# Kernel tuning notes

Hardware: AMD Instinct MI355X
Metric: run time of the kernel (lower is better)

## Reference

```python
import jax, jax.numpy as jnp
import numpy as np

B, L, LE = 2, 1024, 1024
NM, DM, NL = 80, 512, 8
LAYERS = NL // 2
DS, EXP, K, H = 16, 2, 4, 4
DI = EXP * DM            # 1024
DTR = (DM + 15) // 16    # dt_rank 'auto' -> 32
HD = DM // H             # 128


def setup_inputs() -> dict:
    key = jax.random.key(0)
    ks = iter(jax.random.split(key, 48))
    n = lambda shape, s=0.02: jax.random.normal(next(ks), shape, jnp.float32) * s
    return {
        "x": jax.random.normal(next(ks), (B, L, NM), jnp.float32),
        "enc_output": jax.random.normal(next(ks), (B, LE, DM), jnp.float32),
        "W_in": n((DM, NM)), "b_in": jnp.zeros((DM,), jnp.float32),
        "m_norm_w": jnp.ones((LAYERS, DM), jnp.float32),
        "m_in_w": n((LAYERS, 2 * DI, DM)),
        "m_conv_w": n((LAYERS, DI, K), 0.1),
        "m_conv_b": jnp.zeros((LAYERS, DI), jnp.float32),
        "m_xproj_w": n((LAYERS, DTR + 2 * DS, DI)),
        "m_dt_w": n((LAYERS, DI, DTR)),
        "m_dt_b": n((LAYERS, DI), 0.1),
        "m_Alog": jnp.tile(jnp.log(jnp.arange(1, DS + 1, dtype=jnp.float32))[None, None, :], (LAYERS, DI, 1)),
        "m_D": jnp.ones((LAYERS, DI), jnp.float32),
        "m_out_w": n((LAYERS, DM, DI)),
        "a_in_w": n((LAYERS, 3 * DM, DM)),
        "a_in_b": jnp.zeros((LAYERS, 3 * DM), jnp.float32),
        "a_out_w": n((LAYERS, DM, DM)),
        "a_out_b": jnp.zeros((LAYERS, DM), jnp.float32),
        "a_ln_w": jnp.ones((LAYERS, DM), jnp.float32),
        "a_ln_b": jnp.zeros((LAYERS, DM), jnp.float32),
        "normf_w": jnp.ones((DM,), jnp.float32),
        "W_out": n((NM, DM)),
    }


def rmsnorm(x, w, eps=1e-5):
    return x * jax.lax.rsqrt(jnp.mean(x * x, axis=-1, keepdims=True) + eps) * w


def layernorm(x, w, b, eps=1e-5):
    m = jnp.mean(x, axis=-1, keepdims=True)
    v = jnp.mean((x - m) ** 2, axis=-1, keepdims=True)
    return (x - m) * jax.lax.rsqrt(v + eps) * w + b


def dwconv_causal(x, w, b):
    # x: (B,L,DI), w: (DI,K) depthwise; torch Conv1d(padding=K-1)[..., :L] == left-pad K-1
    xt = jnp.transpose(x, (0, 2, 1))  # (B,DI,L)
    y = jax.lax.conv_general_dilated(xt, w[:, None, :], (1,), [(K - 1, 0)],
                                     feature_group_count=DI,
                                     dimension_numbers=("NCH", "OIH", "NCH"))
    return jnp.transpose(y, (0, 2, 1)) + b


def selective_scan_cumsum(u, delta, A, Bm, Cm, Dv):
    # mamba-tiny 'cumsum' scan. u,delta: (B,L,DI); A: (DI,DS); Bm,Cm: (B,L,DS); Dv: (DI,)
    dA = jnp.einsum("bld,dn->bldn", delta, A)
    dBu = jnp.einsum("bld,bld,bln->bldn", delta, u, Bm)
    shifted = jnp.pad(dA[:, 1:], ((0, 0), (0, 1), (0, 0), (0, 0)))
    dA_cs = jnp.exp(jnp.flip(jnp.cumsum(jnp.flip(shifted, 1), 1), 1))  # suffix-sum exp
    xs = jnp.cumsum(dBu * dA_cs, axis=1) / (dA_cs + 1e-12)
    y = jnp.einsum("bldn,bln->bld", xs, Cm)
    return y + u * Dv


def mamba_block(u, in_w, conv_w, conv_b, xproj_w, dt_w, dt_b, Alog, Dv, out_w):
    xr = u @ in_w.T                       # (B,L,2*DI)
    xm, res = xr[..., :DI], xr[..., DI:]
    xm = jax.nn.silu(dwconv_causal(xm, conv_w, conv_b))
    x_dbl = xm @ xproj_w.T                # (B,L,DTR+2*DS)
    dlt = x_dbl[..., :DTR]
    Bm = x_dbl[..., DTR:DTR + DS]
    Cm = x_dbl[..., DTR + DS:]
    delta = jax.nn.softplus(dlt @ dt_w.T + dt_b)
    A = -jnp.exp(Alog)
    y = selective_scan_cumsum(xm, delta, A, Bm, Cm, Dv)
    y = y * jax.nn.silu(res)
    return y @ out_w.T


def cross_attn_block(q_in, kv, in_w, in_b, out_w, out_b, ln_w, ln_b):
    Wq, Wk, Wv = in_w[:DM], in_w[DM:2 * DM], in_w[2 * DM:]
    bq, bk, bv = in_b[:DM], in_b[DM:2 * DM], in_b[2 * DM:]
    q = (q_in @ Wq.T + bq).reshape(B, -1, H, HD)
    k = (kv @ Wk.T + bk).reshape(B, -1, H, HD)
    v = (kv @ Wv.T + bv).reshape(B, -1, H, HD)
    scores = jnp.einsum("bqhd,bkhd->bhqk", q, k) / jnp.sqrt(jnp.float32(HD))
    attn = jax.nn.softmax(scores, axis=-1)
    o = jnp.einsum("bhqk,bkhd->bqhd", attn, v).reshape(B, -1, DM)
    o = o @ out_w.T + out_b
    return layernorm(q_in + o, ln_w, ln_b)  # dropout is identity in eval


def reference(x, enc_output, W_in, b_in, m_norm_w, m_in_w, m_conv_w, m_conv_b,
              m_xproj_w, m_dt_w, m_dt_b, m_Alog, m_D, m_out_w,
              a_in_w, a_in_b, a_out_w, a_out_b, a_ln_w, a_ln_b, normf_w, W_out):
    h = x @ W_in.T + b_in
    for i in range(LAYERS):
        h = h + mamba_block(rmsnorm(h, m_norm_w[i]), m_in_w[i], m_conv_w[i],
                            m_conv_b[i], m_xproj_w[i], m_dt_w[i], m_dt_b[i],
                            m_Alog[i], m_D[i], m_out_w[i])
        h = cross_attn_block(h, enc_output, a_in_w[i], a_in_b[i],
                             a_out_w[i], a_out_b[i], a_ln_w[i], a_ln_b[i])
    h = rmsnorm(h, normf_w)
    return h @ W_out.T
```

## Files before the change

kernel.cpp:

```cpp
#include <hip/hip_runtime.h>
#include <hip/hip_bf16.h>
#include <math.h>

typedef __hip_bfloat16 bf16;
typedef __attribute__((ext_vector_type(8))) short short8x;
typedef __attribute__((ext_vector_type(4))) float f32x4;

static constexpr int cB   = 2;
static constexpr int cL   = 1024;
static constexpr int cLE  = 1024;
static constexpr int cNM  = 80;
static constexpr int cDM  = 512;
static constexpr int cLAYERS = 4;
static constexpr int cDS  = 16;
static constexpr int cKC  = 4;
static constexpr int cH   = 4;
static constexpr int cDI  = 1024;
static constexpr int cDTR = 32;
static constexpr int cHD  = 128;

static constexpr int cNCH = 64;
static constexpr int cCHL = cL / cNCH;
static constexpr int cSPL = 4;

#define GLL16(g, l) __builtin_amdgcn_global_load_lds( \
    (const __attribute__((address_space(1))) void*)(g), \
    (__attribute__((address_space(3))) void*)(l), 16, 0, 0)

template<int ACT, int BM, int BN>
__global__ __launch_bounds__(256)
void bgemm_kernel(const bf16* __restrict__ A, const bf16* __restrict__ W,
                  const float* __restrict__ bias, const float* __restrict__ addv,
                  float* __restrict__ Cf, bf16* __restrict__ Cb,
                  int M, int N, int Kd, int lda, int ldw, int ldcf, int ldcb, int ldadd,
                  int bdiv, long sA1, long sA2, long sW1, long sW2,
                  long sCf1, long sCf2, long sCb1, long sCb2, long sBias)
{
    constexpr int RM = BM / 32;
    constexpr int RN = BN / 32;
    const int z = blockIdx.z;
    const int i1 = z / bdiv, i2 = z % bdiv;
    A += i1 * sA1 + i2 * sA2;
    W += i1 * sW1 + i2 * sW2;
    if (bias) bias += i1 * sBias;

    const int bm = blockIdx.y * BM;
    const int bn = blockIdx.x * BN;
    const int tid = threadIdx.x;
    const int lane = tid & 63;
    const int wid = tid >> 6;
    const int wr = wid >> 1, wc = wid & 1;

    __shared__ bf16 As[BM * 32];
    __shared__ bf16 Bs[BN * 32];

    f32x4 acc[RM][RN] = {};

    const int r_in = lane >> 2;
    const int kb   = (lane & 3) * 8;
    const int hi   = lane >> 4;
    const int rc   = lane & 15;

    for (int k0 = 0; k0 < Kd; k0 += 32) {
#pragma unroll
        for (int iss = 0; iss < BM / 64; iss++) {
            const int row = wid * (BM / 4) + iss * 16 + r_in;
            int gm = bm + row; if (gm >= M) gm = M - 1;
            const bf16* ga = A + (long)gm * lda + k0 + kb;
            GLL16(ga, As + (wid * (BM / 4) + iss * 16) * 32);
        }
#pragma unroll
        for (int iss = 0; iss < BN / 64; iss++) {
            const int row = wid * (BN / 4) + iss * 16 + r_in;
            int gn = bn + row; if (gn >= N) gn = N - 1;
            const bf16* gb = W + (long)gn * ldw + k0 + kb;
            GLL16(gb, Bs + (wid * (BN / 4) + iss * 16) * 32);
        }
        asm volatile("s_waitcnt vmcnt(0)" ::: "memory");
        __syncthreads();

        short8x af[RM], bfv[RN];
#pragma unroll
        for (int i = 0; i < RM; i++)
            af[i] = *(const short8x*)(As + (wr * (BM / 2) + i * 16 + rc) * 32 + hi * 8);
#pragma unroll
        for (int j = 0; j < RN; j++)
            bfv[j] = *(const short8x*)(Bs + (wc * (BN / 2) + j * 16 + rc) * 32 + hi * 8);
#pragma unroll
        for (int i = 0; i < RM; i++)
#pragma unroll
            for (int j = 0; j < RN; j++)
                acc[i][j] = __builtin_amdgcn_mfma_f32_16x16x32_bf16(af[i], bfv[j], acc[i][j], 0, 0, 0);
        __syncthreads();
    }

    const long cfo = i1 * sCf1 + i2 * sCf2;
    const long cbo = i1 * sCb1 + i2 * sCb2;
#pragma unroll
    for (int i = 0; i < RM; i++) {
#pragma unroll
        for (int r = 0; r < 4; r++) {
            const int gm = bm + wr * (BM / 2) + i * 16 + hi * 4 + r;
            if (gm >= M) continue;
#pragma unroll
            for (int j = 0; j < RN; j++) {
                const int gn = bn + wc * (BN / 2) + j * 16 + rc;
                if (gn >= N) continue;
                float v = acc[i][j][r];
                if (bias) v += bias[gn];
                if (ACT == 1) v = (v > 20.f) ? v : log1pf(__expf(v));
                if (addv) v += addv[cfo + (long)gm * ldadd + gn];
                if (Cf) Cf[cfo + (long)gm * ldcf + gn] = v;
                if (Cb) Cb[cbo + (long)gm * ldcb + gn] = __float2bfloat16(v);
            }
        }
    }
}

static inline void bgemm(int ACT, int BM, int BN, const bf16* A, const bf16* W, const float* bias,
                         const float* addv, float* Cf, bf16* Cb,
                         int M, int N, int Kd, int lda, int ldw, int ldcf, int ldcb, int ldadd,
                         int nz, int bdiv, long sA1, long sA2, long sW1, long sW2,
                         long sCf1, long sCf2, long sCb1, long sCb2, long sBias, hipStream_t s)
{
    dim3 g((N + BN - 1) / BN, (M + BM - 1) / BM, nz), b(256);
#define BG_ARGS A, W, bias, addv, Cf, Cb, M, N, Kd, lda, ldw, ldcf, ldcb, ldadd, \
                bdiv, sA1, sA2, sW1, sW2, sCf1, sCf2, sCb1, sCb2, sBias
    if (BM == 128) {
        if (ACT == 1) bgemm_kernel<1, 128, 128><<<g, b, 0, s>>>(BG_ARGS);
        else          bgemm_kernel<0, 128, 128><<<g, b, 0, s>>>(BG_ARGS);
    } else if (BN == 128) {
        if (ACT == 1) bgemm_kernel<1, 64, 128><<<g, b, 0, s>>>(BG_ARGS);
        else          bgemm_kernel<0, 64, 128><<<g, b, 0, s>>>(BG_ARGS);
    } else {
        bgemm_kernel<0, 64, 64><<<g, b, 0, s>>>(BG_ARGS);
    }
#undef BG_ARGS
}

static inline void bgemm_plain(int ACT, int BM, int BN, const bf16* A, const bf16* W,
                               const float* bias, const float* addv, float* Cf, bf16* Cb,
                               int M, int N, int Kd, int lda, int ldw, int ldcf, int ldcb,
                               int ldadd, hipStream_t s)
{
    bgemm(ACT, BM, BN, A, W, bias, addv, Cf, Cb, M, N, Kd, lda, ldw, ldcf, ldcb, ldadd,
          1, 1, 0, 0, 0, 0, 0, 0, 0, 0, 0, s);
}

__global__ __launch_bounds__(128)
void flash_split_kernel(const bf16* __restrict__ Qp, const bf16* __restrict__ Kp,
                        const bf16* __restrict__ VTp, float* __restrict__ OP,
                        float2* __restrict__ ML, float scale)
{
    const int qt = blockIdx.x;
    const int bh = blockIdx.y;
    const int sp = blockIdx.z;
    const int b = bh >> 2, h = bh & 3;
    const int tid = threadIdx.x;
    const int w = tid >> 6;
    const int lane = tid & 63;
    const int rc = lane & 15, hi = lane >> 4;
    const int rlo = rc & 7;

    __shared__ bf16 Ks[64 * 128];
    __shared__ bf16 Vs[128 * 64];
    __shared__ bf16 Ps[32 * 64];

    {
        const bf16* qb = Qp + ((long)(b * cL + qt * 32)) * cDM + h * cHD;
#pragma unroll
        for (int c = 0; c < 4; c++) {
            const int row = w * 16 + c * 4 + (lane >> 4);
            const int gc = (lane & 15) ^ (row & 7);
            GLL16(qb + (long)row * cDM + gc * 8, Ks + (w * 16 + c * 4) * 128);
        }
    }
    asm volatile("s_waitcnt vmcnt(0)" ::: "memory");
    __syncthreads();
    short8x aq[4];
#pragma unroll
    for (int kk = 0; kk < 4; kk++) {
        const int sc = (kk * 4 + hi) ^ rlo;
        aq[kk] = *(const short8x*)(Ks + (w * 16 + rc) * 128 + sc * 8);
    }
    __syncthreads();

    float m_r[4], l_r[4];
#pragma unroll
    for (int r = 0; r < 4; r++) { m_r[r] = -1e30f; l_r[r] = 0.f; }
    f32x4 oacc[8] = {};

    const bf16* kb0 = Kp + ((long)(b * cLE)) * (2 * cDM) + h * cHD;
    const bf16* vb0 = VTp + ((long)(b * cDM + h * cHD)) * cLE;

    for (int t = 0; t < 4; t++) {
        const int kt = sp * 4 + t;
        __syncthreads();
#pragma unroll
        for (int c = 0; c < 8; c++) {
            const int row = w * 32 + c * 4 + (lane >> 4);
            const int gc = (lane & 15) ^ (row & 7);
            GLL16(kb0 + ((long)(kt * 64 + row)) * (2 * cDM) + gc * 8,
                  Ks + (w * 32 + c * 4) * 128);
        }
#pragma unroll
        for (int c = 0; c < 8; c++) {
            const int row = w * 64 + c * 8 + (lane >> 3);
            const int gc = (lane & 7) ^ (row & 7);
            GLL16(vb0 + (long)row * cLE + kt * 64 + gc * 8,
                  Vs + (w * 64 + c * 8) * 64);
        }
        asm volatile("s_waitcnt vmcnt(0)" ::: "memory");
        __syncthreads();

        f32x4 s[4] = {};
#pragma unroll
        for (int kk = 0; kk < 4; kk++) {
            const int sc = (kk * 4 + hi) ^ rlo;
#pragma unroll
            for (int j = 0; j < 4; j++) {
                short8x bk = *(const short8x*)(Ks + (j * 16 + rc) * 128 + sc * 8);
                s[j] = __builtin_amdgcn_mfma_f32_16x16x32_bf16(aq[kk], bk, s[j], 0, 0, 0);
            }
        }

        float p[4][4];
        float esc[4];
#pragma unroll
        for (int r = 0; r < 4; r++) {
            const float v0 = s[0][r] * scale, v1 = s[1][r] * scale;
            const float v2 = s[2][r] * scale, v3 = s[3][r] * scale;
            float mx = fmaxf(fmaxf(v0, v1), fmaxf(v2, v3));
            mx = fmaxf(mx, __shfl_xor(mx, 1));
            mx = fmaxf(mx, __shfl_xor(mx, 2));
            mx = fmaxf(mx, __shfl_xor(mx, 4));
            mx = fmaxf(mx, __shfl_xor(mx, 8));
            const float mn = fmaxf(m_r[r], mx);
            p[0][r] = __expf(v0 - mn);
            p[1][r] = __expf(v1 - mn);
            p[2][r] = __expf(v2 - mn);
            p[3][r] = __expf(v3 - mn);
            float rs = (p[0][r] + p[1][r]) + (p[2][r] + p[3][r]);
            rs += __shfl_xor(rs, 1);
            rs += __shfl_xor(rs, 2);
            rs += __shfl_xor(rs, 4);
            rs += __shfl_xor(rs, 8);
            esc[r] = __expf(m_r[r] - mn);
            l_r[r] = l_r[r] * esc[r] + rs;
            m_r[r] = mn;
        }
#pragma unroll
        for (int j2 = 0; j2 < 8; j2++)
#pragma unroll
            for (int r = 0; r < 4; r++)
                oacc[j2][r] *= esc[r];
#pragma unroll
        for (int j = 0; j < 4; j++)
#pragma unroll
            for (int r = 0; r < 4; r++) {
                const int q = w * 16 + hi * 4 + r;
                const int cp = (j * 2 + (rc >> 3)) ^ (q & 7);
                Ps[q * 64 + cp * 8 + (rc & 7)] = __float2bfloat16(p[j][r]);
            }
        __syncthreads();
#pragma unroll
        for (int ks = 0; ks < 2; ks++) {
            const int sc = (ks * 4 + hi) ^ rlo;
            short8x ap = *(const short8x*)(Ps + (w * 16 + rc) * 64 + sc * 8);
#pragma unroll
            for (int j2 = 0; j2 < 8; j2++) {
                short8x bv = *(const short8x*)(Vs + (j2 * 16 + rc) * 64 + sc * 8);
                oacc[j2] = __builtin_amdgcn_mfma_f32_16x16x32_bf16(ap, bv, oacc[j2], 0, 0, 0);
            }
        }
    }

    float* ob = OP + (((long)sp * (cB * cL) + b * cL + qt * 32)) * cDM + h * cHD;
#pragma unroll
    for (int j2 = 0; j2 < 8; j2++)
#pragma unroll
        for (int r = 0; r < 4; r++)
            ob[(long)(w * 16 + hi * 4 + r) * cDM + j2 * 16 + rc] = oacc[j2][r];
    if (rc == 0) {
#pragma unroll
        for (int r = 0; r < 4; r++) {
            const int row = qt * 32 + w * 16 + hi * 4 + r;
            ML[(((long)sp * cB + b) * cH + h) * cL + row] = make_float2(m_r[r], l_r[r]);
        }
    }
}

__global__ __launch_bounds__(256)
void flash_combine_kernel(const float* __restrict__ OP, const float2* __restrict__ ML,
                          bf16* __restrict__ Op)
{
    const int row = blockIdx.x;
    const int b = row >> 10, lr = row & 1023;
    const int t = threadIdx.x;
    __shared__ float ms[cSPL][cH], ls[cSPL][cH];
    __shared__ float wgt[cSPL][cH], linv[cH];
    if (t < cSPL * cH) {
        const int s = t >> 2, h = t & 3;
        float2 v = ML[(((long)s * cB + b) * cH + h) * cL + lr];
        ms[s][h] = v.x; ls[s][h] = v.y;
    }
    __syncthreads();
    if (t < cH) {
        const int h = t;
        float M = fmaxf(fmaxf(ms[0][h], ms[1][h]), fmaxf(ms[2][h], ms[3][h]));
        float L = 0.f;
#pragma unroll
        for (int s = 0; s < cSPL; s++) {
            const float e = __expf(ms[s][h] - M);
            wgt[s][h] = e;
            L += e * ls[s][h];
        }
        linv[h] = 1.f / L;
    }
    __syncthreads();
#pragma unroll
    for (int c0 = 0; c0 < 2; c0++) {
        const int col = t + c0 * 256;
        const int h = col >> 7;
        float o = 0.f;
#pragma unroll
        for (int s = 0; s < cSPL; s++)
            o += wgt[s][h] * OP[((long)s * (cB * cL) + row) * cDM + col];
        Op[(long)row * cDM + col] = __float2bfloat16(o * linv[h]);
    }
}

__global__ void splitk_reduce_kernel(const float* __restrict__ parts, float* __restrict__ outf,
                                     bf16* __restrict__ outb, int n4, int sliceN4, int S)
{
    const int i = blockIdx.x * 256 + threadIdx.x;
    if (i >= n4) return;
    float4 a = ((const float4*)parts)[i];
    for (int s2 = 1; s2 < S; s2++) {
        float4 b2 = ((const float4*)parts)[i + (long)s2 * sliceN4];
        a.x += b2.x; a.y += b2.y; a.z += b2.z; a.w += b2.w;
    }
    ((float4*)outf)[i] = a;
    bf16 b0 = __float2bfloat16(a.x), b1 = __float2bfloat16(a.y);
    bf16 b2 = __float2bfloat16(a.z), b3 = __float2bfloat16(a.w);
    short4 pk = { *(short*)&b0, *(short*)&b1, *(short*)&b2, *(short*)&b3 };
    ((short4*)outb)[i] = pk;
}

__global__ void cvt_all_kernel(
    const float* __restrict__ s0, bf16* __restrict__ d0,
    const float* __restrict__ s1, bf16* __restrict__ d1,
    const float* __restrict__ s2, bf16* __restrict__ d2,
    const float* __restrict__ s3, bf16* __restrict__ d3,
    const float* __restrict__ s4, bf16* __restrict__ d4,
    const float* __restrict__ s5, bf16* __restrict__ d5,
    const float* __restrict__ s6, bf16* __restrict__ d6,
    const float* __restrict__ s7, bf16* __restrict__ d7)
{
    constexpr long E0 = 1048576, E1 = 4194304, E2 = 262144, E3 = 131072;
    constexpr long E4 = 2097152, E5 = 3145728, E6 = 1048576, E7 = 40960;
    constexpr long C0 = E0, C1 = C0 + E1, C2 = C1 + E2, C3 = C2 + E3;
    constexpr long C4 = C3 + E4, C5 = C4 + E5, C6 = C5 + E6, C7 = C6 + E7;
    long i = ((long)blockIdx.x * 256 + threadIdx.x) * 4;
    if (i >= C7) return;
    const float* s; bf16* d;
    if      (i < C0) { s = s0; d = d0; }
    else if (i < C1) { s = s1; d = d1; i -= C0; }
    else if (i < C2) { s = s2; d = d2; i -= C1; }
    else if (i < C3) { s = s3; d = d3; i -= C2; }
    else if (i < C4) { s = s4; d = d4; i -= C3; }
    else if (i < C5) { s = s5; d = d5; i -= C4; }
    else if (i < C6) { s = s6; d = d6; i -= C5; }
    else             { s = s7; d = d7; i -= C6; }
    float4 v = *(const float4*)(s + i);
    d[i]     = __float2bfloat16(v.x);
    d[i + 1] = __float2bfloat16(v.y);
    d[i + 2] = __float2bfloat16(v.z);
    d[i + 3] = __float2bfloat16(v.w);
}

__global__ void cvt_pad_kernel(const float* __restrict__ in, bf16* __restrict__ out,
                               int rows, int kin, int kout)
{
    const int idx = blockIdx.x * 256 + threadIdx.x;
    if (idx >= rows * kout) return;
    const int r = idx / kout, k = idx - r * kout;
    out[idx] = __float2bfloat16(k < kin ? in[(long)r * kin + k] : 0.f);
}

__global__ void transpose_bf16_kernel(const bf16* __restrict__ in, bf16* __restrict__ out,
                                      int ldin, int col0, long inLS, long outLS)
{
    __shared__ bf16 t[32][33];
    const int z = blockIdx.z;
    const int lay = z >> 1, b = z & 1;
    in  += (long)lay * inLS;
    out += (long)lay * outLS;
    const int le0 = blockIdx.x * 32, d0 = blockIdx.y * 32;
    const int tid = threadIdx.x;
    const int c = tid & 31, r = tid >> 5;
    for (int i = r; i < 32; i += 8)
        t[i][c] = in[((long)b * cLE + le0 + i) * ldin + col0 + d0 + c];
    __syncthreads();
    for (int i = r; i < 32; i += 8)
        out[((long)b * cDM + d0 + i) * cLE + le0 + c] = t[c][i];
}

__global__ void rmsnorm_kernel(const float* __restrict__ x, const float* __restrict__ w,
                               float* __restrict__ outf, bf16* __restrict__ outb, int Dm)
{
    const int row = blockIdx.x;
    const float* xr = x + (long)row * Dm;
    float s = 0.f;
    for (int i = threadIdx.x; i < Dm; i += 256) { float v = xr[i]; s += v * v; }
    __shared__ float red[5];
    const int lane = threadIdx.x & 63, wv = threadIdx.x >> 6;
#pragma unroll
    for (int off = 1; off < 64; off <<= 1) s += __shfl_xor(s, off);
    if (lane == 0) red[wv] = s;
    __syncthreads();
    if (threadIdx.x == 0) {
        float t = red[0] + red[1] + red[2] + red[3];
        red[4] = rsqrtf(t / Dm + 1e-5f);
    }
    __syncthreads();
    const float scale = red[4];
    for (int i = threadIdx.x; i < Dm; i += 256) {
        float v = xr[i] * scale * w[i];
        if (outf) outf[(long)row * Dm + i] = v;
        if (outb) outb[(long)row * Dm + i] = __float2bfloat16(v);
    }
}

__global__ void layernorm_kernel(const float* __restrict__ x, const float* __restrict__ w,
                                 const float* __restrict__ b, float* __restrict__ outf,
                                 bf16* __restrict__ outb,
                                 const float* __restrict__ rms_w, bf16* __restrict__ rms_out)
{
    const int row = blockIdx.x;
    const float* xr = x + (long)row * 512;
    const int t = threadIdx.x;
    const int i0 = t, i1 = t + 256;
    float x0 = xr[i0], x1 = xr[i1];
    float s = x0 + x1, sq = x0 * x0 + x1 * x1;
    __shared__ float red[8];
    __shared__ float mv[2];
    const int lane = t & 63, wv = t >> 6;
#pragma unroll
    for (int off = 1; off < 64; off <<= 1) { s += __shfl_xor(s, off); sq += __shfl_xor(sq, off); }
    if (lane == 0) { red[wv] = s; red[4 + wv] = sq; }
    __syncthreads();
    if (t == 0) {
        float ts = red[0] + red[1] + red[2] + red[3];
        float tq = red[4] + red[5] + red[6] + red[7];
        float m = ts / 512.f;
        float var = tq / 512.f - m * m;
        mv[0] = m;
        mv[1] = rsqrtf(var + 1e-5f);
    }
    __syncthreads();
    const float m = mv[0], rs = mv[1];
    const float v0 = (x0 - m) * rs * w[i0] + b[i0];
    const float v1 = (x1 - m) * rs * w[i1] + b[i1];
    outf[(long)row * 512 + i0] = v0;
    outf[(long)row * 512 + i1] = v1;
    outb[(long)row * 512 + i0] = __float2bfloat16(v0);
    outb[(long)row * 512 + i1] = __float2bfloat16(v1);
    float s2 = v0 * v0 + v1 * v1;
#pragma unroll
    for (int off = 1; off < 64; off <<= 1) s2 += __shfl_xor(s2, off);
    if (lane == 0) red[wv] = s2;
    __syncthreads();
    if (t == 0) mv[0] = rsqrtf((red[0] + red[1] + red[2] + red[3]) / 512.f + 1e-5f);
    __syncthreads();
    const float rsc = mv[0];
    rms_out[(long)row * 512 + i0] = __float2bfloat16(v0 * rsc * rms_w[i0]);
    rms_out[(long)row * 512 + i1] = __float2bfloat16(v1 * rsc * rms_w[i1]);
}

__global__ void conv_silu_kernel(const float* __restrict__ xr, const float* __restrict__ w,
                                 const float* __restrict__ bias, float* __restrict__ xm,
                                 bf16* __restrict__ xmb)
{
    const int idx = blockIdx.x * 256 + threadIdx.x;
    if (idx >= cB * cL * cDI) return;
    const int d = idx & (cDI - 1);
    const int l = (idx >> 10) & (cL - 1);
    const int b = idx >> 20;
    float s = bias[d];
#pragma unroll
    for (int j = 0; j < cKC; j++) {
        const int ls = l + j - (cKC - 1);
        if (ls >= 0) s += w[d * cKC + j] * xr[((long)(b * cL + ls)) * (2 * cDI) + d];
    }
    s = s / (1.f + __expf(-s));
    xm[(long)idx] = s;
    xmb[(long)idx] = __float2bfloat16(s);
}

__global__ void scan_phase1(const float* __restrict__ xm, const float* __restrict__ delta,
                            const float* __restrict__ xdbl, const float* __restrict__ Alog,
                            float* __restrict__ aprod_out, float* __restrict__ send_out)
{
    const int idx4 = blockIdx.x * 256 + threadIdx.x;
    const int ng = idx4 & 3;
    const int d  = (idx4 >> 2) & (cDI - 1);
    const int ch = (idx4 >> 12) & (cNCH - 1);
    const int b  = idx4 >> 18;
    const float4 Al = *(const float4*)(Alog + d * cDS + 4 * ng);
    const float A0 = -__expf(Al.x), A1 = -__expf(Al.y), A2 = -__expf(Al.z), A3 = -__expf(Al.w);
    float s0 = 0.f, s1 = 0.f, s2 = 0.f, s3 = 0.f;
    float p0 = 1.f, p1 = 1.f, p2 = 1.f, p3 = 1.f;
    const int l0 = ch * cCHL;
    const float* dp = delta + (long)(b * cL + l0) * cDI + d;
    const float* up = xm    + (long)(b * cL + l0) * cDI + d;
    const float* xb = xdbl  + (long)(b * cL + l0) * 64 + cDTR + 4 * ng;
#pragma unroll
    for (int t = 0; t < cCHL; t++) {
        const float dl = dp[(long)t * cDI];
        const float du = dl * up[(long)t * cDI];
        const float4 Bv = *(const float4*)(xb + (long)t * 64);
        const float a0 = __expf(dl * A0), a1 = __expf(dl * A1);
        const float a2 = __expf(dl * A2), a3 = __expf(dl * A3);
        s0 = a0 * s0 + du * Bv.x; p0 *= a0;
        s1 = a1 * s1 + du * Bv.y; p1 *= a1;
        s2 = a2 * s2 + du * Bv.z; p2 *= a2;
        s3 = a3 * s3 + du * Bv.w; p3 *= a3;
    }
    const long base4 = (((long)(b * cNCH + ch) * cDI + d) * cDS) + 4 * ng;
    float4 pv = { p0, p1, p2, p3 };
    float4 sv = { s0, s1, s2, s3 };
    *(float4*)(aprod_out + base4) = pv;
    *(float4*)(send_out + base4)  = sv;
}

__global__ void scan_phase2(const float* __restrict__ aprod, const float* __restrict__ send,
                            float* __restrict__ sinit)
{
    const int j = blockIdx.x * 64 + threadIdx.x;
    const int n = j & (cDS - 1);
    const int d = (j >> 4) & (cDI - 1);
    const int b = j >> 14;
    float s = 0.f;
#pragma unroll
    for (int c = 0; c < cNCH; c++) {
        const long off = (((long)(b * cNCH + c) * cDI + d) * cDS) + n;
        sinit[off] = s;
        s = aprod[off] * s + send[off];
    }
}

__global__ void scan_phase3(const float* __restrict__ xm, const float* __restrict__ delta,
                            const float* __restrict__ xdbl, const float* __restrict__ Alog,
                            const float* __restrict__ Dv, const float* __restrict__ xr,
                            const float* __restrict__ sinit, bf16* __restrict__ y)
{
    const int idx4 = blockIdx.x * 256 + threadIdx.x;
    const int ng = idx4 & 3;
    const int d  = (idx4 >> 2) & (cDI - 1);
    const int ch = (idx4 >> 12) & (cNCH - 1);
    const int b  = idx4 >> 18;
    const float4 Al = *(const float4*)(Alog + d * cDS + 4 * ng);
    const float A0 = -__expf(Al.x), A1 = -__expf(Al.y), A2 = -__expf(Al.z), A3 = -__expf(Al.w);
    const float Dval = Dv[d];
    const long base4 = (((long)(b * cNCH + ch) * cDI + d) * cDS) + 4 * ng;
    float4 st = *(const float4*)(sinit + base4);
    float s0 = st.x, s1 = st.y, s2 = st.z, s3 = st.w;
    const int l0 = ch * cCHL;
    const float* dp = delta + (long)(b * cL + l0) * cDI + d;
    const float* up = xm    + (long)(b * cL + l0) * cDI + d;
    const float* xb = xdbl  + (long)(b * cL + l0) * 64 + cDTR + 4 * ng;
    const float* xc = xb + cDS;
    const float* rp = xr + (long)(b * cL + l0) * (2 * cDI) + cDI + d;
    bf16* yp = y + (long)(b * cL + l0) * cDI + d;
#pragma unroll
    for (int t = 0; t < cCHL; t++) {
        const float dl = dp[(long)t * cDI];
        const float u  = up[(long)t * cDI];
        const float du = dl * u;
        const float4 Bv = *(const float4*)(xb + (long)t * 64);
        const float4 Cv = *(const float4*)(xc + (long)t * 64);
        const float a0 = __expf(dl * A0), a1 = __expf(dl * A1);
        const float a2 = __expf(dl * A2), a3 = __expf(dl * A3);
        s0 = a0 * s0 + du * Bv.x;
        s1 = a1 * s1 + du * Bv.y;
        s2 = a2 * s2 + du * Bv.z;
        s3 = a3 * s3 + du * Bv.w;
        float c = s0 * Cv.x;
        c = fmaf(s1, Cv.y, c);
        c = fmaf(s2, Cv.z, c);
        c = fmaf(s3, Cv.w, c);
        c += __shfl_xor(c, 1);
        c += __shfl_xor(c, 2);
        if (ng == 0) {
            const float res = rp[(long)t * 2 * cDI];
            const float sig = 1.f / (1.f + __expf(-res));
            yp[(long)t * cDI] = __float2bfloat16((c + u * Dval) * (res * sig));
        }
    }
}

extern "C" void kernel_launch(void* const* d_in, const int* in_sizes, int n_in,
                              void* d_out, int out_size, void* d_ws, size_t ws_size,
                              hipStream_t stream)
{
    const float* x       = (const float*)d_in[0];
    const float* enc     = (const float*)d_in[1];
    const float* W_in    = (const float*)d_in[2];
    const float* b_in    = (const float*)d_in[3];
    const float* m_norm_w= (const float*)d_in[4];
    const float* m_in_w  = (const float*)d_in[5];
    const float* m_conv_w= (const float*)d_in[6];
    const float* m_conv_b= (const float*)d_in[7];
    const float* m_xproj = (const float*)d_in[8];
    const float* m_dt_w  = (const float*)d_in[9];
    const float* m_dt_b  = (const float*)d_in[10];
    const float* m_Alog  = (const float*)d_in[11];
    const float* m_D     = (const float*)d_in[12];
    const float* m_out_w = (const float*)d_in[13];
    const float* a_in_w  = (const float*)d_in[14];
    const float* a_in_b  = (const float*)d_in[15];
    const float* a_out_w = (const float*)d_in[16];
    const float* a_out_b = (const float*)d_in[17];
    const float* a_ln_w  = (const float*)d_in[18];
    const float* a_ln_b  = (const float*)d_in[19];
    const float* normf_w = (const float*)d_in[20];
    const float* W_out   = (const float*)d_in[21];
    float* out = (float*)d_out;

    float* ws = (float*)d_ws;
    long off = 0;
    auto allocf = [&](long n) { float* p = ws + off; off += n; return p; };

    const long M1 = 1 << 20;
    float* bufH    = allocf(M1);
    float* bufPre  = allocf(M1);
    float* bufXR   = allocf(4 * M1);
    float* bufXM   = allocf(2 * M1);
    float* bufDelta= allocf(2 * M1);
    float* bufXDBL = allocf(M1 / 8);
    bf16* bufU    = (bf16*)allocf(M1 / 2);
    bf16* bufHb   = (bf16*)allocf(M1 / 2);
    bf16* bufXMb  = (bf16*)allocf(M1);
    bf16* bufXDBLb= (bf16*)allocf(M1 / 16);
    bf16* bufY    = (bf16*)allocf(M1);
    bf16* bufQ    = (bf16*)allocf(M1 / 2);
    bf16* bufO    = (bf16*)allocf(M1 / 2);
    bf16* encb    = (bf16*)allocf(M1 / 2);
    bf16* w_in_b  = (bf16*)allocf(2 * M1);
    bf16* w_xp_b  = (bf16*)allocf(M1 / 8);
    bf16* w_dt_b  = (bf16*)allocf(M1 / 16);
    bf16* w_out_b = (bf16*)allocf(M1);
    bf16* w_ain_b = (bf16*)allocf(3 * M1 / 2);
    bf16* w_aout_b= (bf16*)allocf(M1 / 2);
    bf16* x_pad   = (bf16*)allocf(2048L * 96 / 2);
    bf16* w_inp_b = (bf16*)allocf(512L * 96 / 2);
    bf16* w_outf_b= (bf16*)allocf(80L * 512 / 2);
    float* bufAP  = allocf(2 * M1);
    float* bufSE  = allocf(2 * M1);
    float* bufSI  = allocf(2 * M1);
    bf16* bufKV4  = (bf16*)allocf(4 * M1);
    bf16* bufVT4  = (bf16*)allocf(2 * M1);
    float* bufOP  = allocf(4 * M1);
    float2* bufML = (float2*)allocf(M1 / 16);

    const int Mrows = cB * cL;
    const long SUMSZ4 = (long)cB * cNCH * cDI * 4;
    const long kvLS = (long)Mrows * 2 * cDM;
    const long vtLS = (long)cB * cDM * cLE;

    cvt_all_kernel<<<11688, 256, 0, stream>>>(
        enc, encb, m_in_w, w_in_b, m_xproj, w_xp_b, m_dt_w, w_dt_b,
        m_out_w, w_out_b, a_in_w, w_ain_b, a_out_w, w_aout_b, W_out, w_outf_b);
    cvt_pad_kernel<<<(Mrows * 96 + 255) / 256, 256, 0, stream>>>(x, x_pad, Mrows, cNM, 96);
    cvt_pad_kernel<<<(cDM * 96 + 255) / 256, 256, 0, stream>>>(W_in, w_inp_b, cDM, cNM, 96);

    bgemm(0, 64, 128, encb, w_ain_b + (long)cDM * cDM, a_in_b + cDM, nullptr, nullptr, bufKV4,
          Mrows, 2 * cDM, cDM, cDM, cDM, 0, 2 * cDM, 0,
          cLAYERS, 1,
          0, 0,
          (long)3 * cDM * cDM, 0,
          0, 0, kvLS, 0,
          (long)3 * cDM,
          stream);
    {
        dim3 g(cLE / 32, cDM / 32, cLAYERS * cB);
        transpose_bf16_kernel<<<g, 256, 0, stream>>>(bufKV4, bufVT4, 2 * cDM, cDM, kvLS, vtLS);
    }

    bgemm_plain(0, 64, 64, x_pad, w_inp_b, b_in, nullptr, bufH, nullptr,
                Mrows, cDM, 96, 96, 96, cDM, 0, 0, stream);
    rmsnorm_kernel<<<Mrows, 256, 0, stream>>>(bufH, m_norm_w, nullptr, bufU, cDM);

    for (int i = 0; i < cLAYERS; i++) {
        const bf16*  in_w   = w_in_b   + (long)i * 2 * cDI * cDM;
        const float* conv_w = m_conv_w + (long)i * cDI * cKC;
        const float* conv_b = m_conv_b + (long)i * cDI;
        const bf16*  xproj  = w_xp_b   + (long)i * 64 * cDI;
        const bf16*  dt_w   = w_dt_b   + (long)i * cDI * cDTR;
        const float* dt_b   = m_dt_b   + (long)i * cDI;
        const float* Alog   = m_Alog   + (long)i * cDI * cDS;
        const float* Dv     = m_D      + (long)i * cDI;
        const bf16*  out_w  = w_out_b  + (long)i * cDM * cDI;
        const bf16*  ain_w  = w_ain_b  + (long)i * 3 * cDM * cDM;
        const float* ain_b  = a_in_b   + (long)i * 3 * cDM;
        const bf16*  aout_w = w_aout_b + (long)i * cDM * cDM;
        const float* aout_b = a_out_b  + (long)i * cDM;
        const float* ln_w   = a_ln_w   + (long)i * cDM;
        const float* ln_b   = a_ln_b   + (long)i * cDM;
        const bf16*  kv_l   = bufKV4 + (long)i * kvLS;
        const bf16*  vt_l   = bufVT4 + (long)i * vtLS;
        const float* next_rms_w = (i + 1 < cLAYERS) ? (m_norm_w + (long)(i + 1) * cDM) : normf_w;

        bgemm_plain(0, 64, 128, bufU, in_w, nullptr, nullptr, bufXR, nullptr,
                    Mrows, 2 * cDI, cDM, cDM, cDM, 2 * cDI, 0, 0, stream);
        conv_silu_kernel<<<(cB * cL * cDI) / 256, 256, 0, stream>>>(bufXR, conv_w, conv_b, bufXM, bufXMb);
        bgemm(0, 64, 64, bufXMb, xproj, nullptr, nullptr, bufPre, nullptr,
              Mrows, 64, cDI / 8, cDI, cDI, 64, 0, 0,
              8, 1, 128, 0, 128, 0, (long)Mrows * 64, 0, 0, 0, 0, stream);
        splitk_reduce_kernel<<<(Mrows * 64 / 4 + 255) / 256, 256, 0, stream>>>(
            bufPre, bufXDBL, bufXDBLb, Mrows * 64 / 4, Mrows * 64 / 4, 8);
        bgemm_plain(1, 64, 128, bufXDBLb, dt_w, dt_b, nullptr, bufDelta, nullptr,
                    Mrows, cDI, cDTR, 64, cDTR, cDI, 0, 0, stream);
        scan_phase1<<<(int)(SUMSZ4 / 256), 256, 0, stream>>>(bufXM, bufDelta, bufXDBL, Alog, bufAP, bufSE);
        scan_phase2<<<(cB * cDI * cDS) / 64, 64, 0, stream>>>(bufAP, bufSE, bufSI);
        scan_phase3<<<(int)(SUMSZ4 / 256), 256, 0, stream>>>(bufXM, bufDelta, bufXDBL, Alog, Dv, bufXR, bufSI, bufY);
        bgemm_plain(0, 64, 64, bufY, out_w, nullptr, bufH, bufH, bufHb,
                    Mrows, cDM, cDI, cDI, cDI, cDM, cDM, cDM, stream);

        bgemm_plain(0, 64, 64, bufHb, ain_w, ain_b, nullptr, nullptr, bufQ,
                    Mrows, cDM, cDM, cDM, cDM, 0, cDM, 0, stream);
        {
            dim3 g(cL / 32, cB * cH, cSPL);
            flash_split_kernel<<<g, 128, 0, stream>>>(bufQ, kv_l, vt_l, bufOP, bufML,
                                                      0.08838834764831845f);
        }
        flash_combine_kernel<<<Mrows, 256, 0, stream>>>(bufOP, bufML, bufO);
        bgemm_plain(0, 64, 64, bufO, aout_w, aout_b, bufH, bufPre, nullptr,
                    Mrows, cDM, cDM, cDM, cDM, cDM, 0, cDM, stream);
        layernorm_kernel<<<Mrows, 256, 0, stream>>>(bufPre, ln_w, ln_b, bufH, bufHb,
                                                    next_rms_w, bufU);
    }

    bgemm_plain(0, 64, 64, bufU, w_outf_b, nullptr, nullptr, out, nullptr,
                Mrows, cNM, cDM, cDM, cDM, cNM, 0, 0, stream);
}
```

Before: 741.1 us.

## Fuse three chunked selective-scan phases into one kernel with shared-memory prefix scan

```diff
diff --git a/kernel.cpp b/kernel.cpp
--- a/kernel.cpp
+++ b/kernel.cpp
@@ -498,23 +498,33 @@
     xmb[(long)idx] = __float2bfloat16(s);
 }
 
-__global__ void scan_phase1(const float* __restrict__ xm, const float* __restrict__ delta,
-                            const float* __restrict__ xdbl, const float* __restrict__ Alog,
-                            float* __restrict__ aprod_out, float* __restrict__ send_out)
-{
-    const int idx4 = blockIdx.x * 256 + threadIdx.x;
-    const int ng = idx4 & 3;
-    const int d  = (idx4 >> 2) & (cDI - 1);
-    const int ch = (idx4 >> 12) & (cNCH - 1);
-    const int b  = idx4 >> 18;
+__global__ __launch_bounds__(256)
+void scan_fused_kernel(const float* __restrict__ xm, const float* __restrict__ delta,
+                       const float* __restrict__ xdbl, const float* __restrict__ Alog,
+                       const float* __restrict__ Dv, const float* __restrict__ xr,
+                       bf16* __restrict__ y)
+{
+    const int blk = blockIdx.x;
+    const int d = blk & (cDI - 1);
+    const int b = blk >> 10;
+    const int tid = threadIdx.x;
+    const int ch = tid >> 2;
+    const int ng = tid & 3;
+
     const float4 Al = *(const float4*)(Alog + d * cDS + 4 * ng);
     const float A0 = -__expf(Al.x), A1 = -__expf(Al.y), A2 = -__expf(Al.z), A3 = -__expf(Al.w);
-    float s0 = 0.f, s1 = 0.f, s2 = 0.f, s3 = 0.f;
-    float p0 = 1.f, p1 = 1.f, p2 = 1.f, p3 = 1.f;
+    const float Dval = Dv[d];
+
     const int l0 = ch * cCHL;
     const float* dp = delta + (long)(b * cL + l0) * cDI + d;
     const float* up = xm    + (long)(b * cL + l0) * cDI + d;
     const float* xb = xdbl  + (long)(b * cL + l0) * 64 + cDTR + 4 * ng;
+    const float* xc = xb + cDS;
+    const float* rp = xr + (long)(b * cL + l0) * (2 * cDI) + cDI + d;
+    bf16* yp = y + (long)(b * cL + l0) * cDI + d;
+
+    float s0 = 0.f, s1 = 0.f, s2 = 0.f, s3 = 0.f;
+    float p0 = 1.f, p1 = 1.f, p2 = 1.f, p3 = 1.f;
 #pragma unroll
     for (int t = 0; t < cCHL; t++) {
         const float dl = dp[(long)t * cDI];
@@ -527,52 +537,45 @@
         s2 = a2 * s2 + du * Bv.z; p2 *= a2;
         s3 = a3 * s3 + du * Bv.w; p3 *= a3;
     }
-    const long base4 = (((long)(b * cNCH + ch) * cDI + d) * cDS) + 4 * ng;
-    float4 pv = { p0, p1, p2, p3 };
-    float4 sv = { s0, s1, s2, s3 };
-    *(float4*)(aprod_out + base4) = pv;
-    *(float4*)(send_out + base4)  = sv;
-}
-
-__global__ void scan_phase2(const float* __restrict__ aprod, const float* __restrict__ send,
-                            float* __restrict__ sinit)
-{
-    const int j = blockIdx.x * 64 + threadIdx.x;
-    const int n = j & (cDS - 1);
-    const int d = (j >> 4) & (cDI - 1);
-    const int b = j >> 14;
-    float s = 0.f;
-#pragma unroll
-    for (int c = 0; c < cNCH; c++) {
-        const long off = (((long)(b * cNCH + c) * cDI + d) * cDS) + n;
-        sinit[off] = s;
-        s = aprod[off] * s + send[off];
-    }
-}
-
-__global__ void scan_phase3(const float* __restrict__ xm, const float* __restrict__ delta,
-                            const float* __restrict__ xdbl, const float* __restrict__ Alog,
-                            const float* __restrict__ Dv, const float* __restrict__ xr,
-                            const float* __restrict__ sinit, bf16* __restrict__ y)
-{
-    const int idx4 = blockIdx.x * 256 + threadIdx.x;
-    const int ng = idx4 & 3;
-    const int d  = (idx4 >> 2) & (cDI - 1);
-    const int ch = (idx4 >> 12) & (cNCH - 1);
-    const int b  = idx4 >> 18;
-    const float4 Al = *(const float4*)(Alog + d * cDS + 4 * ng);
-    const float A0 = -__expf(Al.x), A1 = -__expf(Al.y), A2 = -__expf(Al.z), A3 = -__expf(Al.w);
-    const float Dval = Dv[d];
-    const long base4 = (((long)(b * cNCH + ch) * cDI + d) * cDS) + 4 * ng;
-    float4 st = *(const float4*)(sinit + base4);
-    float s0 = st.x, s1 = st.y, s2 = st.z, s3 = st.w;
-    const int l0 = ch * cCHL;
-    const float* dp = delta + (long)(b * cL + l0) * cDI + d;
-    const float* up = xm    + (long)(b * cL + l0) * cDI + d;
-    const float* xb = xdbl  + (long)(b * cL + l0) * 64 + cDTR + 4 * ng;
-    const float* xc = xb + cDS;
-    const float* rp = xr + (long)(b * cL + l0) * (2 * cDI) + cDI + d;
-    bf16* yp = y + (long)(b * cL + l0) * cDI + d;
+
+    __shared__ float As[cNCH][17], Ss[cNCH][17];
+    As[ch][4 * ng + 0] = p0; Ss[ch][4 * ng + 0] = s0;
+    As[ch][4 * ng + 1] = p1; Ss[ch][4 * ng + 1] = s1;
+    As[ch][4 * ng + 2] = p2; Ss[ch][4 * ng + 2] = s2;
+    As[ch][4 * ng + 3] = p3; Ss[ch][4 * ng + 3] = s3;
+    __syncthreads();
+    for (int st = 1; st < cNCH; st <<= 1) {
+        float na[4], nb[4];
+        const bool act = (ch >= st);
+        if (act) {
+#pragma unroll
+            for (int j = 0; j < 4; j++) {
+                const int n = 4 * ng + j;
+                const float ah = As[ch][n], bh = Ss[ch][n];
+                na[j] = ah * As[ch - st][n];
+                nb[j] = ah * Ss[ch - st][n] + bh;
+            }
+        }
+        __syncthreads();
+        if (act) {
+#pragma unroll
+            for (int j = 0; j < 4; j++) {
+                const int n = 4 * ng + j;
+                As[ch][n] = na[j];
+                Ss[ch][n] = nb[j];
+            }
+        }
+        __syncthreads();
+    }
+    if (ch > 0) {
+        s0 = Ss[ch - 1][4 * ng + 0];
+        s1 = Ss[ch - 1][4 * ng + 1];
+        s2 = Ss[ch - 1][4 * ng + 2];
+        s3 = Ss[ch - 1][4 * ng + 3];
+    } else {
+        s0 = s1 = s2 = s3 = 0.f;
+    }
+
 #pragma unroll
     for (int t = 0; t < cCHL; t++) {
         const float dl = dp[(long)t * cDI];
@@ -656,16 +659,12 @@
     bf16* x_pad   = (bf16*)allocf(2048L * 96 / 2);
     bf16* w_inp_b = (bf16*)allocf(512L * 96 / 2);
     bf16* w_outf_b= (bf16*)allocf(80L * 512 / 2);
-    float* bufAP  = allocf(2 * M1);
-    float* bufSE  = allocf(2 * M1);
-    float* bufSI  = allocf(2 * M1);
     bf16* bufKV4  = (bf16*)allocf(4 * M1);
     bf16* bufVT4  = (bf16*)allocf(2 * M1);
     float* bufOP  = allocf(4 * M1);
     float2* bufML = (float2*)allocf(M1 / 16);
 
     const int Mrows = cB * cL;
-    const long SUMSZ4 = (long)cB * cNCH * cDI * 4;
     const long kvLS = (long)Mrows * 2 * cDM;
     const long vtLS = (long)cB * cDM * cLE;
 
@@ -722,9 +721,8 @@
             bufPre, bufXDBL, bufXDBLb, Mrows * 64 / 4, Mrows * 64 / 4, 8);
         bgemm_plain(1, 64, 128, bufXDBLb, dt_w, dt_b, nullptr, bufDelta, nullptr,
                     Mrows, cDI, cDTR, 64, cDTR, cDI, 0, 0, stream);
-        scan_phase1<<<(int)(SUMSZ4 / 256), 256, 0, stream>>>(bufXM, bufDelta, bufXDBL, Alog, bufAP, bufSE);
-        scan_phase2<<<(cB * cDI * cDS) / 64, 64, 0, stream>>>(bufAP, bufSE, bufSI);
-        scan_phase3<<<(int)(SUMSZ4 / 256), 256, 0, stream>>>(bufXM, bufDelta, bufXDBL, Alog, Dv, bufXR, bufSI, bufY);
+        scan_fused_kernel<<<cB * cDI, 256, 0, stream>>>(bufXM, bufDelta, bufXDBL, Alog, Dv,
+                                                        bufXR, bufY);
         bgemm_plain(0, 64, 64, bufY, out_w, nullptr, bufH, bufH, bufHb,
                     Mrows, cDM, cDI, cDI, cDI, cDM, cDM, cDM, stream);
 
```

Result: slower. 912.2 us (+23.1%).

## Give each scan thread all 16 states and vectorize conv-silu by four channels

Applied to the files above, without the earlier changes.

```diff
diff --git a/kernel.cpp b/kernel.cpp
--- a/kernel.cpp
+++ b/kernel.cpp
@@ -483,55 +483,82 @@
                                  bf16* __restrict__ xmb)
 {
     const int idx = blockIdx.x * 256 + threadIdx.x;
-    if (idx >= cB * cL * cDI) return;
-    const int d = idx & (cDI - 1);
-    const int l = (idx >> 10) & (cL - 1);
-    const int b = idx >> 20;
-    float s = bias[d];
+    const int d4 = idx & (cDI / 4 - 1);
+    const int l  = (idx >> 8) & (cL - 1);
+    const int b  = idx >> 18;
+    const int d  = d4 * 4;
+    float4 acc = *(const float4*)(bias + d);
+    float w0a[4], w1a[4], w2a[4], w3a[4];
+    *(float4*)w0a = *(const float4*)(w + (d + 0) * cKC);
+    *(float4*)w1a = *(const float4*)(w + (d + 1) * cKC);
+    *(float4*)w2a = *(const float4*)(w + (d + 2) * cKC);
+    *(float4*)w3a = *(const float4*)(w + (d + 3) * cKC);
 #pragma unroll
     for (int j = 0; j < cKC; j++) {
         const int ls = l + j - (cKC - 1);
-        if (ls >= 0) s += w[d * cKC + j] * xr[((long)(b * cL + ls)) * (2 * cDI) + d];
-    }
-    s = s / (1.f + __expf(-s));
-    xm[(long)idx] = s;
-    xmb[(long)idx] = __float2bfloat16(s);
-}
-
-__global__ void scan_phase1(const float* __restrict__ xm, const float* __restrict__ delta,
-                            const float* __restrict__ xdbl, const float* __restrict__ Alog,
-                            float* __restrict__ aprod_out, float* __restrict__ send_out)
-{
-    const int idx4 = blockIdx.x * 256 + threadIdx.x;
-    const int ng = idx4 & 3;
-    const int d  = (idx4 >> 2) & (cDI - 1);
-    const int ch = (idx4 >> 12) & (cNCH - 1);
-    const int b  = idx4 >> 18;
-    const float4 Al = *(const float4*)(Alog + d * cDS + 4 * ng);
-    const float A0 = -__expf(Al.x), A1 = -__expf(Al.y), A2 = -__expf(Al.z), A3 = -__expf(Al.w);
-    float s0 = 0.f, s1 = 0.f, s2 = 0.f, s3 = 0.f;
-    float p0 = 1.f, p1 = 1.f, p2 = 1.f, p3 = 1.f;
+        if (ls >= 0) {
+            const float4 xv = *(const float4*)(xr + ((long)(b * cL + ls)) * (2 * cDI) + d);
+            acc.x = fmaf(w0a[j], xv.x, acc.x);
+            acc.y = fmaf(w1a[j], xv.y, acc.y);
+            acc.z = fmaf(w2a[j], xv.z, acc.z);
+            acc.w = fmaf(w3a[j], xv.w, acc.w);
+        }
+    }
+    acc.x = acc.x / (1.f + __expf(-acc.x));
+    acc.y = acc.y / (1.f + __expf(-acc.y));
+    acc.z = acc.z / (1.f + __expf(-acc.z));
+    acc.w = acc.w / (1.f + __expf(-acc.w));
+    const long o = ((long)(b * cL + l)) * cDI + d;
+    *(float4*)(xm + o) = acc;
+    bf16 b0 = __float2bfloat16(acc.x), b1 = __float2bfloat16(acc.y);
+    bf16 b2 = __float2bfloat16(acc.z), b3 = __float2bfloat16(acc.w);
+    short4 pk = { *(short*)&b0, *(short*)&b1, *(short*)&b2, *(short*)&b3 };
+    *(short4*)(xmb + o) = pk;
+}
+
+__global__ __launch_bounds__(256)
+void scan_phase1(const float* __restrict__ xm, const float* __restrict__ delta,
+                 const float* __restrict__ xdbl, const float* __restrict__ Alog,
+                 float* __restrict__ aprod_out, float* __restrict__ send_out)
+{
+    const int idx = blockIdx.x * 256 + threadIdx.x;
+    const int d  = idx & (cDI - 1);
+    const int ch = (idx >> 10) & (cNCH - 1);
+    const int b  = idx >> 16;
+    float A[16], s[16], p[16];
+#pragma unroll
+    for (int g = 0; g < 4; g++) {
+        const float4 v = *(const float4*)(Alog + d * cDS + 4 * g);
+        A[4 * g + 0] = -__expf(v.x); A[4 * g + 1] = -__expf(v.y);
+        A[4 * g + 2] = -__expf(v.z); A[4 * g + 3] = -__expf(v.w);
+    }
+#pragma unroll
+    for (int n = 0; n < 16; n++) { s[n] = 0.f; p[n] = 1.f; }
     const int l0 = ch * cCHL;
     const float* dp = delta + (long)(b * cL + l0) * cDI + d;
     const float* up = xm    + (long)(b * cL + l0) * cDI + d;
-    const float* xb = xdbl  + (long)(b * cL + l0) * 64 + cDTR + 4 * ng;
+    const float* xb = xdbl  + (long)(b * cL + l0) * 64 + cDTR;
 #pragma unroll
     for (int t = 0; t < cCHL; t++) {
         const float dl = dp[(long)t * cDI];
         const float du = dl * up[(long)t * cDI];
-        const float4 Bv = *(const float4*)(xb + (long)t * 64);
-        const float a0 = __expf(dl * A0), a1 = __expf(dl * A1);
-        const float a2 = __expf(dl * A2), a3 = __expf(dl * A3);
-        s0 = a0 * s0 + du * Bv.x; p0 *= a0;
-        s1 = a1 * s1 + du * Bv.y; p1 *= a1;
-        s2 = a2 * s2 + du * Bv.z; p2 *= a2;
-        s3 = a3 * s3 + du * Bv.w; p3 *= a3;
-    }
-    const long base4 = (((long)(b * cNCH + ch) * cDI + d) * cDS) + 4 * ng;
-    float4 pv = { p0, p1, p2, p3 };
-    float4 sv = { s0, s1, s2, s3 };
-    *(float4*)(aprod_out + base4) = pv;
-    *(float4*)(send_out + base4)  = sv;
+#pragma unroll
+        for (int g = 0; g < 4; g++) {
+            const float4 Bv = *(const float4*)(xb + (long)t * 64 + 4 * g);
+            float a;
+            a = __expf(dl * A[4 * g + 0]); s[4 * g + 0] = fmaf(du, Bv.x, a * s[4 * g + 0]); p[4 * g + 0] *= a;
+            a = __expf(dl * A[4 * g + 1]); s[4 * g + 1] = fmaf(du, Bv.y, a * s[4 * g + 1]); p[4 * g + 1] *= a;
+            a = __expf(dl * A[4 * g + 2]); s[4 * g + 2] = fmaf(du, Bv.z, a * s[4 * g + 2]); p[4 * g + 2] *= a;
+            a = __expf(dl * A[4 * g + 3]); s[4 * g + 3] = fmaf(du, Bv.w, a * s[4 * g + 3]); p[4 * g + 3] *= a;
+        }
+    }
+    float* pa = aprod_out + (((long)(b * cNCH + ch) * cDI + d) * cDS);
+    float* ps = send_out  + (((long)(b * cNCH + ch) * cDI + d) * cDS);
+#pragma unroll
+    for (int g = 0; g < 4; g++) {
+        *(float4*)(pa + 4 * g) = make_float4(p[4 * g], p[4 * g + 1], p[4 * g + 2], p[4 * g + 3]);
+        *(float4*)(ps + 4 * g) = make_float4(s[4 * g], s[4 * g + 1], s[4 * g + 2], s[4 * g + 3]);
+    }
 }
 
 __global__ void scan_phase2(const float* __restrict__ aprod, const float* __restrict__ send,
@@ -550,27 +577,34 @@
     }
 }
 
-__global__ void scan_phase3(const float* __restrict__ xm, const float* __restrict__ delta,
-                            const float* __restrict__ xdbl, const float* __restrict__ Alog,
-                            const float* __restrict__ Dv, const float* __restrict__ xr,
-                            const float* __restrict__ sinit, bf16* __restrict__ y)
-{
-    const int idx4 = blockIdx.x * 256 + threadIdx.x;
-    const int ng = idx4 & 3;
-    const int d  = (idx4 >> 2) & (cDI - 1);
-    const int ch = (idx4 >> 12) & (cNCH - 1);
-    const int b  = idx4 >> 18;
-    const float4 Al = *(const float4*)(Alog + d * cDS + 4 * ng);
-    const float A0 = -__expf(Al.x), A1 = -__expf(Al.y), A2 = -__expf(Al.z), A3 = -__expf(Al.w);
+__global__ __launch_bounds__(256)
+void scan_phase3(const float* __restrict__ xm, const float* __restrict__ delta,
+                 const float* __restrict__ xdbl, const float* __restrict__ Alog,
+                 const float* __restrict__ Dv, const float* __restrict__ xr,
+                 const float* __restrict__ sinit, bf16* __restrict__ y)
+{
+    const int idx = blockIdx.x * 256 + threadIdx.x;
+    const int d  = idx & (cDI - 1);
+    const int ch = (idx >> 10) & (cNCH - 1);
+    const int b  = idx >> 16;
+    float A[16], s[16];
+#pragma unroll
+    for (int g = 0; g < 4; g++) {
+        const float4 v = *(const float4*)(Alog + d * cDS + 4 * g);
+        A[4 * g + 0] = -__expf(v.x); A[4 * g + 1] = -__expf(v.y);
+        A[4 * g + 2] = -__expf(v.z); A[4 * g + 3] = -__expf(v.w);
+    }
     const float Dval = Dv[d];
-    const long base4 = (((long)(b * cNCH + ch) * cDI + d) * cDS) + 4 * ng;
-    float4 st = *(const float4*)(sinit + base4);
-    float s0 = st.x, s1 = st.y, s2 = st.z, s3 = st.w;
+    const float* si = sinit + (((long)(b * cNCH + ch) * cDI + d) * cDS);
+#pragma unroll
+    for (int g = 0; g < 4; g++) {
+        const float4 v = *(const float4*)(si + 4 * g);
+        s[4 * g + 0] = v.x; s[4 * g + 1] = v.y; s[4 * g + 2] = v.z; s[4 * g + 3] = v.w;
+    }
     const int l0 = ch * cCHL;
     const float* dp = delta + (long)(b * cL + l0) * cDI + d;
     const float* up = xm    + (long)(b * cL + l0) * cDI + d;
-    const float* xb = xdbl  + (long)(b * cL + l0) * 64 + cDTR + 4 * ng;
-    const float* xc = xb + cDS;
+    const float* xb = xdbl  + (long)(b * cL + l0) * 64 + cDTR;
     const float* rp = xr + (long)(b * cL + l0) * (2 * cDI) + cDI + d;
     bf16* yp = y + (long)(b * cL + l0) * cDI + d;
 #pragma unroll
@@ -578,25 +612,20 @@
         const float dl = dp[(long)t * cDI];
         const float u  = up[(long)t * cDI];
         const float du = dl * u;
-        const float4 Bv = *(const float4*)(xb + (long)t * 64);
-        const float4 Cv = *(const float4*)(xc + (long)t * 64);
-        const float a0 = __expf(dl * A0), a1 = __expf(dl * A1);
-        const float a2 = __expf(dl * A2), a3 = __expf(dl * A3);
-        s0 = a0 * s0 + du * Bv.x;
-        s1 = a1 * s1 + du * Bv.y;
-        s2 = a2 * s2 + du * Bv.z;
-        s3 = a3 * s3 + du * Bv.w;
-        float c = s0 * Cv.x;
-        c = fmaf(s1, Cv.y, c);
-        c = fmaf(s2, Cv.z, c);
-        c = fmaf(s3, Cv.w, c);
-        c += __shfl_xor(c, 1);
-        c += __shfl_xor(c, 2);
-        if (ng == 0) {
-            const float res = rp[(long)t * 2 * cDI];
-            const float sig = 1.f / (1.f + __expf(-res));
-            yp[(long)t * cDI] = __float2bfloat16((c + u * Dval) * (res * sig));
-        }
+        float c = 0.f;
+#pragma unroll
+        for (int g = 0; g < 4; g++) {
+            const float4 Bv = *(const float4*)(xb + (long)t * 64 + 4 * g);
+            const float4 Cv = *(const float4*)(xb + (long)t * 64 + cDS + 4 * g);
+            float a;
+            a = __expf(dl * A[4 * g + 0]); s[4 * g + 0] = fmaf(du, Bv.x, a * s[4 * g + 0]); c = fmaf(s[4 * g + 0], Cv.x, c);
+            a = __expf(dl * A[4 * g + 1]); s[4 * g + 1] = fmaf(du, Bv.y, a * s[4 * g + 1]); c = fmaf(s[4 * g + 1], Cv.y, c);
+            a = __expf(dl * A[4 * g + 2]); s[4 * g + 2] = fmaf(du, Bv.z, a * s[4 * g + 2]); c = fmaf(s[4 * g + 2], Cv.z, c);
+            a = __expf(dl * A[4 * g + 3]); s[4 * g + 3] = fmaf(du, Bv.w, a * s[4 * g + 3]); c = fmaf(s[4 * g + 3], Cv.w, c);
+        }
+        const float res = rp[(long)t * 2 * cDI];
+        const float sig = 1.f / (1.f + __expf(-res));
+        yp[(long)t * cDI] = __float2bfloat16((c + u * Dval) * (res * sig));
     }
 }
 
@@ -665,7 +694,7 @@
     float2* bufML = (float2*)allocf(M1 / 16);
 
     const int Mrows = cB * cL;
-    const long SUMSZ4 = (long)cB * cNCH * cDI * 4;
+    const int scanBlocks = (cB * cNCH * cDI) / 256;
     const long kvLS = (long)Mrows * 2 * cDM;
     const long vtLS = (long)cB * cDM * cLE;
 
@@ -714,7 +743,7 @@
 
         bgemm_plain(0, 64, 128, bufU, in_w, nullptr, nullptr, bufXR, nullptr,
                     Mrows, 2 * cDI, cDM, cDM, cDM, 2 * cDI, 0, 0, stream);
-        conv_silu_kernel<<<(cB * cL * cDI) / 256, 256, 0, stream>>>(bufXR, conv_w, conv_b, bufXM, bufXMb);
+        conv_silu_kernel<<<(cB * cL * cDI / 4) / 256, 256, 0, stream>>>(bufXR, conv_w, conv_b, bufXM, bufXMb);
         bgemm(0, 64, 64, bufXMb, xproj, nullptr, nullptr, bufPre, nullptr,
               Mrows, 64, cDI / 8, cDI, cDI, 64, 0, 0,
               8, 1, 128, 0, 128, 0, (long)Mrows * 64, 0, 0, 0, 0, stream);
@@ -722,9 +751,9 @@
             bufPre, bufXDBL, bufXDBLb, Mrows * 64 / 4, Mrows * 64 / 4, 8);
         bgemm_plain(1, 64, 128, bufXDBLb, dt_w, dt_b, nullptr, bufDelta, nullptr,
                     Mrows, cDI, cDTR, 64, cDTR, cDI, 0, 0, stream);
-        scan_phase1<<<(int)(SUMSZ4 / 256), 256, 0, stream>>>(bufXM, bufDelta, bufXDBL, Alog, bufAP, bufSE);
+        scan_phase1<<<scanBlocks, 256, 0, stream>>>(bufXM, bufDelta, bufXDBL, Alog, bufAP, bufSE);
         scan_phase2<<<(cB * cDI * cDS) / 64, 64, 0, stream>>>(bufAP, bufSE, bufSI);
-        scan_phase3<<<(int)(SUMSZ4 / 256), 256, 0, stream>>>(bufXM, bufDelta, bufXDBL, Alog, Dv, bufXR, bufSI, bufY);
+        scan_phase3<<<scanBlocks, 256, 0, stream>>>(bufXM, bufDelta, bufXDBL, Alog, Dv, bufXR, bufSI, bufY);
         bgemm_plain(0, 64, 64, bufY, out_w, nullptr, bufH, bufH, bufHb,
                     Mrows, cDM, cDI, cDI, cDI, cDM, cDM, cDM, stream);
 
```

Result: faster. 714.3 us (median of 2 runs) (-3.6%).
